# Performance work log

Measured on AMD Instinct MI355X. Metric: run time of the kernel, lower is better.

## Reference

```python
import jax, jax.numpy as jnp
import numpy as np

NUM_HEADS = 16
NEG = -1e10


def setup_inputs() -> dict:
    key = jax.random.key(0)
    ks = jax.random.split(key, 5)
    S, E = 2048, 2048
    scale_in = 1.0 / np.sqrt(E)
    return {
        "x": jax.random.normal(ks[0], (S, E), dtype=jnp.float32),
        "W_attn": jax.random.normal(ks[1], (E, 3 * E), dtype=jnp.float32) * scale_in,
        "b_attn": jax.random.normal(ks[2], (3 * E,), dtype=jnp.float32) * 0.02,
        "W_proj": jax.random.normal(ks[3], (E, E), dtype=jnp.float32) * scale_in,
        "b_proj": jax.random.normal(ks[4], (E,), dtype=jnp.float32) * 0.02,
    }


def reference(x, W_attn, b_attn, W_proj, b_proj):
    S, E = x.shape
    H = NUM_HEADS
    D = E // H
    # c_attn: [S, 3E]
    h = x @ W_attn + b_attn
    # view(S, 3, -1).transpose(0,1) -> [3, S, E]; then view(3, S, H, D).transpose(1,2) -> [3, H, S, D]
    qkv = h.reshape(S, 3, E).transpose(1, 0, 2)          # [3, S, E]
    q, k, v = qkv.reshape(3, S, H, D).transpose(0, 2, 1, 3)  # each [H, S, D]
    # causal mask: (1 - tril) * -1e10, added before softmax
    mask = (1.0 - jnp.tril(jnp.ones((S, S), dtype=x.dtype))) * NEG
    scores = jnp.einsum("hsd,htd->hst", q, k) / jnp.sqrt(jnp.asarray(D, dtype=x.dtype))
    attn = jax.nn.softmax(scores + mask, axis=-1)
    out_heads = jnp.einsum("hst,htd->hsd", attn, v)      # [H, S, D]
    # hstack over heads == transpose to [S, H, D] then flatten to [S, E]
    concat = out_heads.transpose(1, 0, 2).reshape(S, E)
    out = concat @ W_proj + b_proj
    # current_cache = (k, v) pre-head-split: [S, E] each
    return out, qkv[1], qkv[2]
```

## Files before the change

### kernel.cpp

```cpp
#include <hip/hip_runtime.h>
#include <hip/hip_bf16.h>
#include <stdint.h>

#define S_DIM 2048
#define E_DIM 2048
#define H_NUM 16
#define D_HEAD 128
#define N3E 6144

typedef __attribute__((ext_vector_type(8))) short short8;
typedef __attribute__((ext_vector_type(4))) float f32x4;
typedef __attribute__((ext_vector_type(8))) unsigned short ushort8;

__device__ __forceinline__ unsigned short f32_to_bf16_bits(float f) {
    __hip_bfloat16 b = __float2bfloat16(f);
    unsigned short u;
    __builtin_memcpy(&u, &b, 2);
    return u;
}
__device__ __forceinline__ float bf16_bits_to_f32(unsigned short u) {
    unsigned int v = ((unsigned int)u) << 16;
    float f;
    __builtin_memcpy(&f, &v, 4);
    return f;
}

__global__ void k_convert(const float* __restrict__ in, __hip_bfloat16* __restrict__ out, int n) {
    int i = (blockIdx.x * 256 + threadIdx.x) * 8;
    if (i >= n) return;
    float4 a = *(const float4*)(in + i);
    float4 b = *(const float4*)(in + i + 4);
    ushort8 o;
    o[0] = f32_to_bf16_bits(a.x);
    o[1] = f32_to_bf16_bits(a.y);
    o[2] = f32_to_bf16_bits(a.z);
    o[3] = f32_to_bf16_bits(a.w);
    o[4] = f32_to_bf16_bits(b.x);
    o[5] = f32_to_bf16_bits(b.y);
    o[6] = f32_to_bf16_bits(b.z);
    o[7] = f32_to_bf16_bits(b.w);
    *(ushort8*)(out + i) = o;
}

__global__ void k_transpose_convert(const float* __restrict__ in, __hip_bfloat16* __restrict__ out,
                                    int R, int C) {
    __shared__ float tile[32][33];
    int c0 = blockIdx.x * 32, r0 = blockIdx.y * 32;
    int tx = threadIdx.x, ty = threadIdx.y;
#pragma unroll
    for (int i = 0; i < 4; ++i) {
        int r = r0 + ty + i * 8;
        tile[ty + i * 8][tx] = in[(size_t)r * C + c0 + tx];
    }
    __syncthreads();
#pragma unroll
    for (int i = 0; i < 4; ++i) {
        int c = c0 + ty + i * 8;
        out[(size_t)c * R + r0 + tx] = __float2bfloat16(tile[tx][ty + i * 8]);
    }
}

__global__ void k_transpose_v(const __hip_bfloat16* __restrict__ qkv, __hip_bfloat16* __restrict__ vT) {
    __shared__ __hip_bfloat16 tile[32][33];
    int c0 = blockIdx.x * 32, t0 = blockIdx.y * 32;
    int tx = threadIdx.x, ty = threadIdx.y;
#pragma unroll
    for (int i = 0; i < 4; ++i) {
        int t = t0 + ty + i * 8;
        tile[ty + i * 8][tx] = qkv[(size_t)t * N3E + 2 * E_DIM + c0 + tx];
    }
    __syncthreads();
#pragma unroll
    for (int i = 0; i < 4; ++i) {
        int c = c0 + ty + i * 8;
        vT[(size_t)c * S_DIM + t0 + tx] = tile[tx][ty + i * 8];
    }
}

template <int EPI>
__global__ __launch_bounds__(512, 2) void k_gemm256(const __hip_bfloat16* __restrict__ A,
                                                    const __hip_bfloat16* __restrict__ Bt,
                                                    const float* __restrict__ bias,
                                                    float* __restrict__ outF,
                                                    __hip_bfloat16* __restrict__ outB,
                                                    int M, int N, int K) {
    __shared__ __hip_bfloat16 As[4][256 * 32];
    __shared__ __hip_bfloat16 Bs[4][256 * 32];

    const int tid = threadIdx.x;
    const int w = tid >> 6, lane = tid & 63;
    const int lg = lane >> 4, l16 = lane & 15;
    const int wr = w >> 2, wc = w & 3;
    const int ntx = N >> 8;
    const int chunk = ((M >> 8) * ntx) >> 3;
    const int lin = blockIdx.x;
    const int swz = (lin & 7) * chunk + (lin >> 3);
    const int m0 = (swz / ntx) << 8, n0 = (swz % ntx) << 8;
    const int NT = K >> 5;

    const int srow = tid >> 2;
    const int scol = ((tid & 3) ^ ((tid >> 3) & 3)) * 8;
    const __hip_bfloat16* aB = A + (size_t)(m0 + srow) * K + scol;
    const __hip_bfloat16* bB = Bt + (size_t)(n0 + srow) * K + scol;
    const size_t rstep = (size_t)128 * K;

#define STAGE(u, p)                                                                                   \
    do {                                                                                              \
        __builtin_amdgcn_global_load_lds(                                                             \
            (const __attribute__((address_space(1))) void*)(aB + (p) * rstep + (u) * 32),             \
            (__attribute__((address_space(3))) void*)(&As[(u) & 3][(p) * 4096 + tid * 8]), 16, 0, 0); \
        __builtin_amdgcn_global_load_lds(                                                             \
            (const __attribute__((address_space(1))) void*)(bB + (p) * rstep + (u) * 32),             \
            (__attribute__((address_space(3))) void*)(&Bs[(u) & 3][(p) * 4096 + tid * 8]), 16, 0, 0); \
    } while (0)

    f32x4 acc[8][4];
#pragma unroll
    for (int i = 0; i < 8; ++i)
#pragma unroll
        for (int j = 0; j < 4; ++j) acc[i][j] = {0.f, 0.f, 0.f, 0.f};

    STAGE(0, 0); STAGE(0, 1);
    STAGE(1, 0); STAGE(1, 1);
    STAGE(2, 0); STAGE(2, 1);
    asm volatile("s_waitcnt vmcnt(8)" ::: "memory");
    __builtin_amdgcn_s_barrier();

    short8 af[4], bf[4];
    for (int t = 0; t < NT; ++t) {
        const int cur = t & 3;
        const int u = t + 3;
#pragma unroll
        for (int i = 0; i < 4; ++i) {
            int arow = wr * 128 + i * 16 + l16;
            af[i] = *(const short8*)&As[cur][arow * 32 + ((lg ^ ((arow >> 1) & 3)) * 8)];
            int brow = wc * 64 + i * 16 + l16;
            bf[i] = *(const short8*)&Bs[cur][brow * 32 + ((lg ^ ((brow >> 1) & 3)) * 8)];
        }
        if (u < NT) { STAGE(u, 0); STAGE(u, 1); }
        __builtin_amdgcn_s_setprio(1);
#pragma unroll
        for (int mi = 0; mi < 4; ++mi)
#pragma unroll
            for (int ni = 0; ni < 4; ++ni)
                acc[mi][ni] = __builtin_amdgcn_mfma_f32_16x16x32_bf16(af[mi], bf[ni], acc[mi][ni], 0, 0, 0);
        __builtin_amdgcn_s_setprio(0);
#pragma unroll
        for (int i = 0; i < 4; ++i) {
            int arow = wr * 128 + 64 + i * 16 + l16;
            af[i] = *(const short8*)&As[cur][arow * 32 + ((lg ^ ((arow >> 1) & 3)) * 8)];
        }
        __builtin_amdgcn_s_setprio(1);
#pragma unroll
        for (int mi = 0; mi < 4; ++mi)
#pragma unroll
            for (int ni = 0; ni < 4; ++ni)
                acc[4 + mi][ni] = __builtin_amdgcn_mfma_f32_16x16x32_bf16(af[mi], bf[ni], acc[4 + mi][ni], 0, 0, 0);
        __builtin_amdgcn_s_setprio(0);
        __builtin_amdgcn_sched_barrier(0);
        if (t < NT - 3)
            asm volatile("s_waitcnt vmcnt(8)" ::: "memory");
        else if (t == NT - 3)
            asm volatile("s_waitcnt vmcnt(4)" ::: "memory");
        else if (t == NT - 2)
            asm volatile("s_waitcnt vmcnt(0)" ::: "memory");
        __builtin_amdgcn_sched_barrier(0);
        __builtin_amdgcn_s_barrier();
    }
#undef STAGE

    const size_t OFF_K = (size_t)S_DIM * E_DIM;
    const size_t OFF_V = 2 * (size_t)S_DIM * E_DIM;
#pragma unroll
    for (int ni = 0; ni < 4; ++ni) {
        int jcol = n0 + wc * 64 + ni * 16 + l16;
        float bj = bias[jcol];
#pragma unroll
        for (int mi = 0; mi < 8; ++mi) {
#pragma unroll
            for (int r = 0; r < 4; ++r) {
                int s = m0 + wr * 128 + mi * 16 + lg * 4 + r;
                float v = acc[mi][ni][r] + bj;
                if (EPI == 1) {
                    outB[(size_t)s * N + jcol] = __float2bfloat16(v);
                    if (jcol >= 2 * E_DIM) {
                        outF[OFF_V + (size_t)s * E_DIM + (jcol - 2 * E_DIM)] = v;
                    } else if (jcol >= E_DIM) {
                        outF[OFF_K + (size_t)s * E_DIM + (jcol - E_DIM)] = v;
                    }
                } else {
                    outF[(size_t)s * N + jcol] = v;
                }
            }
        }
    }
}

template <int EPI>
__global__ __launch_bounds__(256, 2) void k_gemm128(const __hip_bfloat16* __restrict__ A,
                                                    const __hip_bfloat16* __restrict__ Bt,
                                                    const float* __restrict__ bias,
                                                    float* __restrict__ outF,
                                                    __hip_bfloat16* __restrict__ outB,
                                                    int M, int N, int K) {
    __shared__ __hip_bfloat16 As[4][128 * 32];
    __shared__ __hip_bfloat16 Bs[4][128 * 32];

    const int tid = threadIdx.x;
    const int w = tid >> 6, lane = tid & 63;
    const int lg = lane >> 4, l16 = lane & 15;
    const int wr = w >> 1, wc = w & 1;
    const int ntx = N >> 7;
    const int chunk = ((M >> 7) * ntx) >> 3;
    const int lin = blockIdx.x;
    const int swz = (lin & 7) * chunk + (lin >> 3);
    const int m0 = (swz / ntx) << 7, n0 = (swz % ntx) << 7;
    const int NT = K >> 5;

    const int srow = tid >> 2;
    const int scol = ((tid & 3) ^ ((tid >> 3) & 3)) * 8;
    const __hip_bfloat16* aB = A + (size_t)(m0 + srow) * K + scol;
    const __hip_bfloat16* bB = Bt + (size_t)(n0 + srow) * K + scol;
    const size_t rstep = (size_t)64 * K;

#define STG(u, p)                                                                                     \
    do {                                                                                              \
        __builtin_amdgcn_global_load_lds(                                                             \
            (const __attribute__((address_space(1))) void*)(aB + (p) * rstep + (u) * 32),             \
            (__attribute__((address_space(3))) void*)(&As[(u) & 3][(p) * 2048 + tid * 8]), 16, 0, 0); \
        __builtin_amdgcn_global_load_lds(                                                             \
            (const __attribute__((address_space(1))) void*)(bB + (p) * rstep + (u) * 32),             \
            (__attribute__((address_space(3))) void*)(&Bs[(u) & 3][(p) * 2048 + tid * 8]), 16, 0, 0); \
    } while (0)

    f32x4 acc[4][4];
#pragma unroll
    for (int i = 0; i < 4; ++i)
#pragma unroll
        for (int j = 0; j < 4; ++j) acc[i][j] = {0.f, 0.f, 0.f, 0.f};

    STG(0, 0); STG(0, 1);
    STG(1, 0); STG(1, 1);
    STG(2, 0); STG(2, 1);
    asm volatile("s_waitcnt vmcnt(8)" ::: "memory");
    __builtin_amdgcn_s_barrier();

    short8 af[4], bfr[4];
    for (int t = 0; t < NT; ++t) {
        const int cur = t & 3;
        const int u = t + 3;
#pragma unroll
        for (int i = 0; i < 4; ++i) {
            int arow = wr * 64 + i * 16 + l16;
            af[i] = *(const short8*)&As[cur][arow * 32 + ((lg ^ ((arow >> 1) & 3)) * 8)];
            int brow = wc * 64 + i * 16 + l16;
            bfr[i] = *(const short8*)&Bs[cur][brow * 32 + ((lg ^ ((brow >> 1) & 3)) * 8)];
        }
        if (u < NT) { STG(u, 0); STG(u, 1); }
        __builtin_amdgcn_s_setprio(1);
#pragma unroll
        for (int mi = 0; mi < 4; ++mi)
#pragma unroll
            for (int ni = 0; ni < 4; ++ni)
                acc[mi][ni] = __builtin_amdgcn_mfma_f32_16x16x32_bf16(af[mi], bfr[ni], acc[mi][ni], 0, 0, 0);
        __builtin_amdgcn_s_setprio(0);
        __builtin_amdgcn_sched_barrier(0);
        if (t < NT - 3)
            asm volatile("s_waitcnt vmcnt(8)" ::: "memory");
        else if (t == NT - 3)
            asm volatile("s_waitcnt vmcnt(4)" ::: "memory");
        else if (t == NT - 2)
            asm volatile("s_waitcnt vmcnt(0)" ::: "memory");
        __builtin_amdgcn_sched_barrier(0);
        __builtin_amdgcn_s_barrier();
    }
#undef STG

    const size_t OFF_K = (size_t)S_DIM * E_DIM;
    const size_t OFF_V = 2 * (size_t)S_DIM * E_DIM;
#pragma unroll
    for (int ni = 0; ni < 4; ++ni) {
        int jcol = n0 + wc * 64 + ni * 16 + l16;
        float bj = bias[jcol];
#pragma unroll
        for (int mi = 0; mi < 4; ++mi) {
#pragma unroll
            for (int r = 0; r < 4; ++r) {
                int s = m0 + wr * 64 + mi * 16 + lg * 4 + r;
                float v = acc[mi][ni][r] + bj;
                if (EPI == 1) {
                    outB[(size_t)s * N + jcol] = __float2bfloat16(v);
                    if (jcol >= 2 * E_DIM) {
                        outF[OFF_V + (size_t)s * E_DIM + (jcol - 2 * E_DIM)] = v;
                    } else if (jcol >= E_DIM) {
                        outF[OFF_K + (size_t)s * E_DIM + (jcol - E_DIM)] = v;
                    }
                } else {
                    outF[(size_t)s * N + jcol] = v;
                }
            }
        }
    }
}

__global__ __launch_bounds__(256) void k_attn(const __hip_bfloat16* __restrict__ qkv,
                                              const __hip_bfloat16* __restrict__ vT,
                                              __hip_bfloat16* __restrict__ concat,
                                              __hip_bfloat16* __restrict__ Ob,
                                              float* __restrict__ ml) {
    const int h = blockIdx.y;
    const int xs = 47 - (int)blockIdx.x;
    int x, tstart, tend, chunk = 0;
    bool split;
    if (xs < 16) {
        x = xs; tstart = 0; tend = x + 1; split = false;
    } else {
        int idx = xs - 16;
        x = 16 + (idx >> 1);
        chunk = idx & 1;
        int L = x + 1, half = L >> 1;
        tstart = chunk ? half : 0;
        tend = chunk ? L : half;
        split = true;
    }
    const int q0 = x * 64;
    const int tid = threadIdx.x;
    const int w = tid >> 6, lane = tid & 63;
    const int lg = lane >> 4, l16 = lane & 15;
    const int sbase = q0 + w * 16;
    const float scale = 0.08838834764831845f;
    const float FIXM = 8.0f;

    __shared__ __hip_bfloat16 Ks[2][64 * 128];
    __shared__ __hip_bfloat16 Vs[2][128 * 64];
    __shared__ __hip_bfloat16 plds[4][16 * 84];

    short8 qa[4];
#pragma unroll
    for (int kc = 0; kc < 4; ++kc)
        qa[kc] = *(const short8*)&qkv[(size_t)(sbase + l16) * N3E + h * D_HEAD + kc * 32 + lg * 8];

    short8 ones;
#pragma unroll
    for (int j = 0; j < 8; ++j) ones[j] = (short)0x3F80;

    f32x4 O[8];
#pragma unroll
    for (int i = 0; i < 8; ++i) O[i] = {0.f, 0.f, 0.f, 0.f};
    f32x4 accL = {0.f, 0.f, 0.f, 0.f};

    auto stage = [&](int buf, int it) {
        const int t0 = it * 64;
#pragma unroll
        for (int j = 0; j < 4; ++j) {
            int kr = j * 16 + w * 4 + (lane >> 4);
            int ks16 = (lane & 15) ^ (kr & 7);
            const __hip_bfloat16* gk = qkv + (size_t)(t0 + kr) * N3E + E_DIM + h * D_HEAD + ks16 * 8;
            __builtin_amdgcn_global_load_lds((const __attribute__((address_space(1))) void*)gk,
                                             (__attribute__((address_space(3))) void*)(&Ks[buf][j * 2048 + w * 512]),
                                             16, 0, 0);
            int vd = j * 32 + w * 8 + (lane >> 3);
            int vs16 = (lane & 7) ^ (vd & 7);
            const __hip_bfloat16* gv = vT + (size_t)(h * D_HEAD + vd) * S_DIM + t0 + vs16 * 8;
            __builtin_amdgcn_global_load_lds((const __attribute__((address_space(1))) void*)gv,
                                             (__attribute__((address_space(3))) void*)(&Vs[buf][j * 2048 + w * 512]),
                                             16, 0, 0);
        }
    };

    stage(0, tstart);
    int cur = 0;

    for (int it = tstart; it < tend; ++it) {
        const int t0 = it * 64;
        __syncthreads();
        if (it + 1 < tend) stage(cur ^ 1, it + 1);
        const bool diag = (t0 == q0);

        f32x4 sc[4];
        __builtin_amdgcn_s_setprio(1);
#pragma unroll
        for (int f = 0; f < 4; ++f) {
            sc[f] = {0.f, 0.f, 0.f, 0.f};
            int r = f * 16 + l16;
#pragma unroll
            for (int kc = 0; kc < 4; ++kc) {
                int ce = (kc * 32 + lg * 8) ^ ((r & 7) << 3);
                short8 kb = *(const short8*)&Ks[cur][r * 128 + ce];
                sc[f] = __builtin_amdgcn_mfma_f32_16x16x32_bf16(qa[kc], kb, sc[f], 0, 0, 0);
            }
        }
        __builtin_amdgcn_s_setprio(0);

#pragma unroll
        for (int f = 0; f < 4; ++f) {
#pragma unroll
            for (int r = 0; r < 4; ++r) {
                float v = sc[f][r] * scale - FIXM;
                if (diag) {
                    int t = t0 + f * 16 + l16;
                    int s = sbase + lg * 4 + r;
                    if (t > s) v = -1e30f;
                }
                sc[f][r] = __expf(v);
            }
        }

#pragma unroll
        for (int f = 0; f < 4; ++f)
#pragma unroll
            for (int r = 0; r < 4; ++r)
                plds[w][(lg * 4 + r) * 84 + f * 16 + l16] = __float2bfloat16(sc[f][r]);
        short8 pa[2];
#pragma unroll
        for (int tc = 0; tc < 2; ++tc)
            pa[tc] = *(const short8*)&plds[w][l16 * 84 + tc * 32 + lg * 8];

        __builtin_amdgcn_s_setprio(1);
        accL = __builtin_amdgcn_mfma_f32_16x16x32_bf16(pa[0], ones, accL, 0, 0, 0);
        accL = __builtin_amdgcn_mfma_f32_16x16x32_bf16(pa[1], ones, accL, 0, 0, 0);
#pragma unroll
        for (int f2 = 0; f2 < 8; ++f2) {
            int d = f2 * 16 + l16;
#pragma unroll
            for (int tc = 0; tc < 2; ++tc) {
                int ce = (tc * 32 + lg * 8) ^ ((d & 7) << 3);
                short8 vb = *(const short8*)&Vs[cur][d * 64 + ce];
                O[f2] = __builtin_amdgcn_mfma_f32_16x16x32_bf16(pa[tc], vb, O[f2], 0, 0, 0);
            }
        }
        __builtin_amdgcn_s_setprio(0);
        cur ^= 1;
    }

    if (!split) {
#pragma unroll
        for (int f2 = 0; f2 < 8; ++f2) {
#pragma unroll
            for (int r = 0; r < 4; ++r) {
                int s = sbase + lg * 4 + r;
                float v = O[f2][r] / accL[r];
                concat[(size_t)s * E_DIM + h * D_HEAD + f2 * 16 + l16] = __float2bfloat16(v);
            }
        }
    } else {
        const int sub = (h * 16 + (x - 16)) * 2 + chunk;
#pragma unroll
        for (int f2 = 0; f2 < 8; ++f2) {
#pragma unroll
            for (int r = 0; r < 4; ++r) {
                int row = w * 16 + lg * 4 + r;
                Ob[(size_t)sub * 8192 + row * 128 + f2 * 16 + l16] = __float2bfloat16(O[f2][r]);
            }
        }
        if (l16 == 0) {
#pragma unroll
            for (int r = 0; r < 4; ++r) {
                int row = w * 16 + lg * 4 + r;
                ml[((size_t)sub * 64 + row) * 2 + 0] = FIXM;
                ml[((size_t)sub * 64 + row) * 2 + 1] = accL[r];
            }
        }
    }
}

__global__ __launch_bounds__(256) void k_combine(const __hip_bfloat16* __restrict__ Ob,
                                                 const float* __restrict__ ml,
                                                 __hip_bfloat16* __restrict__ concat) {
    const int xx = blockIdx.x;
    const int h = blockIdx.y;
    const int tid = threadIdx.x;
    const int row = tid >> 2;
    const int d0 = (tid & 3) * 32;
    const int sub0 = (h * 16 + xx) * 2, sub1 = sub0 + 1;
    const float m0 = ml[((size_t)sub0 * 64 + row) * 2 + 0];
    const float l0 = ml[((size_t)sub0 * 64 + row) * 2 + 1];
    const float m1 = ml[((size_t)sub1 * 64 + row) * 2 + 0];
    const float l1 = ml[((size_t)sub1 * 64 + row) * 2 + 1];
    const float M = fmaxf(m0, m1);
    const float w0 = __expf(m0 - M), w1 = __expf(m1 - M);
    const float inv = 1.f / (w0 * l0 + w1 * l1);
    const int s = (xx + 16) * 64 + row;
#pragma unroll
    for (int j = 0; j < 32; j += 8) {
        ushort8 a = *(const ushort8*)&Ob[(size_t)sub0 * 8192 + row * 128 + d0 + j];
        ushort8 b = *(const ushort8*)&Ob[(size_t)sub1 * 8192 + row * 128 + d0 + j];
        ushort8 o;
#pragma unroll
        for (int q = 0; q < 8; ++q) {
            float fa = bf16_bits_to_f32(a[q]);
            float fb = bf16_bits_to_f32(b[q]);
            o[q] = f32_to_bf16_bits((w0 * fa + w1 * fb) * inv);
        }
        *(ushort8*)&concat[(size_t)s * E_DIM + h * D_HEAD + d0 + j] = o;
    }
}

extern "C" void kernel_launch(void* const* d_in, const int* in_sizes, int n_in,
                              void* d_out, int out_size, void* d_ws, size_t ws_size,
                              hipStream_t stream) {
    const float* x = (const float*)d_in[0];
    const float* W_attn = (const float*)d_in[1];
    const float* b_attn = (const float*)d_in[2];
    const float* W_proj = (const float*)d_in[3];
    const float* b_proj = (const float*)d_in[4];
    float* out = (float*)d_out;

    __hip_bfloat16* xb = (__hip_bfloat16*)d_ws;
    __hip_bfloat16* WaT = xb + (size_t)S_DIM * E_DIM;
    __hip_bfloat16* WpT = WaT + (size_t)N3E * E_DIM;
    __hip_bfloat16* qkvb = WpT + (size_t)E_DIM * E_DIM;
    __hip_bfloat16* vT = qkvb + (size_t)S_DIM * N3E;
    __hip_bfloat16* concat = xb;
    __hip_bfloat16* Ob = WaT;
    float* ml = (float*)(WaT + (size_t)512 * 8192);

    k_convert<<<dim3((S_DIM * E_DIM) / (256 * 8)), dim3(256), 0, stream>>>(x, xb, S_DIM * E_DIM);
    k_transpose_convert<<<dim3(N3E / 32, E_DIM / 32), dim3(32, 8), 0, stream>>>(W_attn, WaT, E_DIM, N3E);
    k_transpose_convert<<<dim3(E_DIM / 32, E_DIM / 32), dim3(32, 8), 0, stream>>>(W_proj, WpT, E_DIM, E_DIM);
    k_gemm256<1><<<dim3(192), dim3(512), 0, stream>>>(xb, WaT, b_attn, out, qkvb, S_DIM, N3E, E_DIM);
    k_transpose_v<<<dim3(E_DIM / 32, S_DIM / 32), dim3(32, 8), 0, stream>>>(qkvb, vT);
    k_attn<<<dim3(48, H_NUM), dim3(256), 0, stream>>>(qkvb, vT, concat, Ob, ml);
    k_combine<<<dim3(16, H_NUM), dim3(256), 0, stream>>>(Ob, ml, concat);
    k_gemm128<0><<<dim3(256), dim3(256), 0, stream>>>(concat, WpT, b_proj, out, nullptr,
                                                      S_DIM, E_DIM, E_DIM);
}
```

Before: 206.3 us.

## Restructure QKV GEMM into double-buffered 64-wide K steps with split A/B staging

Rewrites the pipeline of the 256x256 QKV projection GEMM. The 4-deep ring of 32-wide K tiles becomes a double buffer of 64-wide K tiles split into two halves. A and B prefetches are interleaved between four MFMA sub-phases, each separated by barriers, and the 2D launch grid replaces the swizzled 1D block order. The aim is better overlap of global-to-LDS loads with MFMA work and deeper per-iteration compute. It adds many more barriers per iteration and drops the L2-friendly tile swizzle, which could hurt cache reuse.

```diff
diff --git a/kernel.cpp b/kernel.cpp
--- a/kernel.cpp
+++ b/kernel.cpp
@@ -11,6 +11,10 @@
 typedef __attribute__((ext_vector_type(8))) short short8;
 typedef __attribute__((ext_vector_type(4))) float f32x4;
 typedef __attribute__((ext_vector_type(8))) unsigned short ushort8;
+
+#define GLD16(src, dst)                                                          \
+    __builtin_amdgcn_global_load_lds((const __attribute__((address_space(1))) void*)(src), \
+                                     (__attribute__((address_space(3))) void*)(dst), 16, 0, 0)
 
 __device__ __forceinline__ unsigned short f32_to_bf16_bits(float f) {
     __hip_bfloat16 b = __float2bfloat16(f);
@@ -84,35 +88,38 @@
                                                     float* __restrict__ outF,
                                                     __hip_bfloat16* __restrict__ outB,
                                                     int M, int N, int K) {
-    __shared__ __hip_bfloat16 As[4][256 * 32];
-    __shared__ __hip_bfloat16 Bs[4][256 * 32];
+    __shared__ __hip_bfloat16 As[2][2][256 * 32];
+    __shared__ __hip_bfloat16 Bs[2][2][256 * 32];
 
     const int tid = threadIdx.x;
     const int w = tid >> 6, lane = tid & 63;
     const int lg = lane >> 4, l16 = lane & 15;
     const int wr = w >> 2, wc = w & 3;
-    const int ntx = N >> 8;
-    const int chunk = ((M >> 8) * ntx) >> 3;
-    const int lin = blockIdx.x;
-    const int swz = (lin & 7) * chunk + (lin >> 3);
-    const int m0 = (swz / ntx) << 8, n0 = (swz % ntx) << 8;
-    const int NT = K >> 5;
-
-    const int srow = tid >> 2;
-    const int scol = ((tid & 3) ^ ((tid >> 3) & 3)) * 8;
-    const __hip_bfloat16* aB = A + (size_t)(m0 + srow) * K + scol;
-    const __hip_bfloat16* bB = Bt + (size_t)(n0 + srow) * K + scol;
-    const size_t rstep = (size_t)128 * K;
-
-#define STAGE(u, p)                                                                                   \
-    do {                                                                                              \
-        __builtin_amdgcn_global_load_lds(                                                             \
-            (const __attribute__((address_space(1))) void*)(aB + (p) * rstep + (u) * 32),             \
-            (__attribute__((address_space(3))) void*)(&As[(u) & 3][(p) * 4096 + tid * 8]), 16, 0, 0); \
-        __builtin_amdgcn_global_load_lds(                                                             \
-            (const __attribute__((address_space(1))) void*)(bB + (p) * rstep + (u) * 32),             \
-            (__attribute__((address_space(3))) void*)(&Bs[(u) & 3][(p) * 4096 + tid * 8]), 16, 0, 0); \
-    } while (0)
+    const int m0 = blockIdx.y * 256, n0 = blockIdx.x * 256;
+    const int NT = K >> 6;
+
+    int srow[2], sk16[2];
+#pragma unroll
+    for (int j = 0; j < 2; ++j) {
+        int slot = j * 512 + tid;
+        srow[j] = slot >> 2;
+        sk16[j] = (tid & 3) ^ ((slot >> 3) & 3);
+    }
+
+    auto stageA = [&](int buf, int kh, int t) {
+#pragma unroll
+        for (int j = 0; j < 2; ++j) {
+            const __hip_bfloat16* g = A + (size_t)(m0 + srow[j]) * K + t * 64 + kh * 32 + sk16[j] * 8;
+            GLD16(g, &As[buf][kh][(j * 512 + tid) * 8]);
+        }
+    };
+    auto stageB = [&](int buf, int kh, int t) {
+#pragma unroll
+        for (int j = 0; j < 2; ++j) {
+            const __hip_bfloat16* g = Bt + (size_t)(n0 + srow[j]) * K + t * 64 + kh * 32 + sk16[j] * 8;
+            GLD16(g, &Bs[buf][kh][(j * 512 + tid) * 8]);
+        }
+    };
 
     f32x4 acc[8][4];
 #pragma unroll
@@ -120,54 +127,107 @@
 #pragma unroll
         for (int j = 0; j < 4; ++j) acc[i][j] = {0.f, 0.f, 0.f, 0.f};
 
-    STAGE(0, 0); STAGE(0, 1);
-    STAGE(1, 0); STAGE(1, 1);
-    STAGE(2, 0); STAGE(2, 1);
-    asm volatile("s_waitcnt vmcnt(8)" ::: "memory");
+    stageA(0, 0, 0);
+    stageB(0, 0, 0);
+    stageA(0, 1, 0);
+    stageB(0, 1, 0);
+    asm volatile("s_waitcnt vmcnt(4)" ::: "memory");
     __builtin_amdgcn_s_barrier();
 
-    short8 af[4], bf[4];
     for (int t = 0; t < NT; ++t) {
-        const int cur = t & 3;
-        const int u = t + 3;
-#pragma unroll
-        for (int i = 0; i < 4; ++i) {
-            int arow = wr * 128 + i * 16 + l16;
-            af[i] = *(const short8*)&As[cur][arow * 32 + ((lg ^ ((arow >> 1) & 3)) * 8)];
-            int brow = wc * 64 + i * 16 + l16;
-            bf[i] = *(const short8*)&Bs[cur][brow * 32 + ((lg ^ ((brow >> 1) & 3)) * 8)];
-        }
-        if (u < NT) { STAGE(u, 0); STAGE(u, 1); }
-        __builtin_amdgcn_s_setprio(1);
-#pragma unroll
-        for (int mi = 0; mi < 4; ++mi)
-#pragma unroll
-            for (int ni = 0; ni < 4; ++ni)
-                acc[mi][ni] = __builtin_amdgcn_mfma_f32_16x16x32_bf16(af[mi], bf[ni], acc[mi][ni], 0, 0, 0);
-        __builtin_amdgcn_s_setprio(0);
-#pragma unroll
-        for (int i = 0; i < 4; ++i) {
-            int arow = wr * 128 + 64 + i * 16 + l16;
-            af[i] = *(const short8*)&As[cur][arow * 32 + ((lg ^ ((arow >> 1) & 3)) * 8)];
-        }
-        __builtin_amdgcn_s_setprio(1);
-#pragma unroll
-        for (int mi = 0; mi < 4; ++mi)
-#pragma unroll
-            for (int ni = 0; ni < 4; ++ni)
-                acc[4 + mi][ni] = __builtin_amdgcn_mfma_f32_16x16x32_bf16(af[mi], bf[ni], acc[4 + mi][ni], 0, 0, 0);
-        __builtin_amdgcn_s_setprio(0);
-        __builtin_amdgcn_sched_barrier(0);
-        if (t < NT - 3)
-            asm volatile("s_waitcnt vmcnt(8)" ::: "memory");
-        else if (t == NT - 3)
-            asm volatile("s_waitcnt vmcnt(4)" ::: "memory");
-        else if (t == NT - 2)
-            asm volatile("s_waitcnt vmcnt(0)" ::: "memory");
-        __builtin_amdgcn_sched_barrier(0);
-        __builtin_amdgcn_s_barrier();
-    }
-#undef STAGE
+        const int cur = t & 1;
+        const int nt = (t + 1 < NT) ? t + 1 : t;
+        const int nb = (t + 1) & 1;
+        short8 af[8], bp0[2], bp1[2];
+
+#pragma unroll
+        for (int mi = 0; mi < 8; ++mi) {
+            int row = wr * 128 + mi * 16 + l16;
+            af[mi] = *(const short8*)&As[cur][0][row * 32 + ((lg ^ ((row >> 1) & 3)) * 8)];
+        }
+#pragma unroll
+        for (int p = 0; p < 2; ++p) {
+            int row = wc * 64 + p * 16 + l16;
+            bp0[p] = *(const short8*)&Bs[cur][0][row * 32 + ((lg ^ ((row >> 1) & 3)) * 8)];
+        }
+        stageA(nb, 0, nt);
+        __builtin_amdgcn_s_barrier();
+        asm volatile("s_waitcnt lgkmcnt(0)" ::: "memory");
+        __builtin_amdgcn_sched_barrier(0);
+        __builtin_amdgcn_s_setprio(1);
+#pragma unroll
+        for (int mi = 0; mi < 8; ++mi)
+#pragma unroll
+            for (int p = 0; p < 2; ++p)
+                acc[mi][p] = __builtin_amdgcn_mfma_f32_16x16x32_bf16(af[mi], bp0[p], acc[mi][p], 0, 0, 0);
+        __builtin_amdgcn_s_setprio(0);
+        __builtin_amdgcn_s_barrier();
+
+#pragma unroll
+        for (int p = 0; p < 2; ++p) {
+            int row = wc * 64 + (2 + p) * 16 + l16;
+            bp1[p] = *(const short8*)&Bs[cur][0][row * 32 + ((lg ^ ((row >> 1) & 3)) * 8)];
+        }
+        stageB(nb, 0, nt);
+        __builtin_amdgcn_s_barrier();
+        asm volatile("s_waitcnt lgkmcnt(0)" ::: "memory");
+        __builtin_amdgcn_sched_barrier(0);
+        __builtin_amdgcn_s_setprio(1);
+#pragma unroll
+        for (int mi = 0; mi < 8; ++mi)
+#pragma unroll
+            for (int p = 0; p < 2; ++p)
+                acc[mi][2 + p] = __builtin_amdgcn_mfma_f32_16x16x32_bf16(af[mi], bp1[p], acc[mi][2 + p], 0, 0, 0);
+        __builtin_amdgcn_s_setprio(0);
+        __builtin_amdgcn_sched_barrier(0);
+        asm volatile("s_waitcnt vmcnt(4)" ::: "memory");
+        __builtin_amdgcn_sched_barrier(0);
+        __builtin_amdgcn_s_barrier();
+
+#pragma unroll
+        for (int mi = 0; mi < 8; ++mi) {
+            int row = wr * 128 + mi * 16 + l16;
+            af[mi] = *(const short8*)&As[cur][1][row * 32 + ((lg ^ ((row >> 1) & 3)) * 8)];
+        }
+#pragma unroll
+        for (int p = 0; p < 2; ++p) {
+            int row = wc * 64 + p * 16 + l16;
+            bp0[p] = *(const short8*)&Bs[cur][1][row * 32 + ((lg ^ ((row >> 1) & 3)) * 8)];
+        }
+        stageA(nb, 1, nt);
+        __builtin_amdgcn_s_barrier();
+        asm volatile("s_waitcnt lgkmcnt(0)" ::: "memory");
+        __builtin_amdgcn_sched_barrier(0);
+        __builtin_amdgcn_s_setprio(1);
+#pragma unroll
+        for (int mi = 0; mi < 8; ++mi)
+#pragma unroll
+            for (int p = 0; p < 2; ++p)
+                acc[mi][p] = __builtin_amdgcn_mfma_f32_16x16x32_bf16(af[mi], bp0[p], acc[mi][p], 0, 0, 0);
+        __builtin_amdgcn_s_setprio(0);
+        __builtin_amdgcn_s_barrier();
+
+#pragma unroll
+        for (int p = 0; p < 2; ++p) {
+            int row = wc * 64 + (2 + p) * 16 + l16;
+            bp1[p] = *(const short8*)&Bs[cur][1][row * 32 + ((lg ^ ((row >> 1) & 3)) * 8)];
+        }
+        stageB(nb, 1, nt);
+        __builtin_amdgcn_s_barrier();
+        asm volatile("s_waitcnt lgkmcnt(0)" ::: "memory");
+        __builtin_amdgcn_sched_barrier(0);
+        __builtin_amdgcn_s_setprio(1);
+#pragma unroll
+        for (int mi = 0; mi < 8; ++mi)
+#pragma unroll
+            for (int p = 0; p < 2; ++p)
+                acc[mi][2 + p] = __builtin_amdgcn_mfma_f32_16x16x32_bf16(af[mi], bp1[p], acc[mi][2 + p], 0, 0, 0);
+        __builtin_amdgcn_s_setprio(0);
+        __builtin_amdgcn_sched_barrier(0);
+        asm volatile("s_waitcnt vmcnt(4)" ::: "memory");
+        __builtin_amdgcn_sched_barrier(0);
+        __builtin_amdgcn_s_barrier();
+    }
 
     const size_t OFF_K = (size_t)S_DIM * E_DIM;
     const size_t OFF_V = 2 * (size_t)S_DIM * E_DIM;
@@ -225,12 +285,8 @@
 
 #define STG(u, p)                                                                                     \
     do {                                                                                              \
-        __builtin_amdgcn_global_load_lds(                                                             \
-            (const __attribute__((address_space(1))) void*)(aB + (p) * rstep + (u) * 32),             \
-            (__attribute__((address_space(3))) void*)(&As[(u) & 3][(p) * 2048 + tid * 8]), 16, 0, 0); \
-        __builtin_amdgcn_global_load_lds(                                                             \
-            (const __attribute__((address_space(1))) void*)(bB + (p) * rstep + (u) * 32),             \
-            (__attribute__((address_space(3))) void*)(&Bs[(u) & 3][(p) * 2048 + tid * 8]), 16, 0, 0); \
+        GLD16(aB + (p) * rstep + (u) * 32, &As[(u) & 3][(p) * 2048 + tid * 8]);                       \
+        GLD16(bB + (p) * rstep + (u) * 32, &Bs[(u) & 3][(p) * 2048 + tid * 8]);                       \
     } while (0)
 
     f32x4 acc[4][4];
@@ -356,15 +412,11 @@
             int kr = j * 16 + w * 4 + (lane >> 4);
             int ks16 = (lane & 15) ^ (kr & 7);
             const __hip_bfloat16* gk = qkv + (size_t)(t0 + kr) * N3E + E_DIM + h * D_HEAD + ks16 * 8;
-            __builtin_amdgcn_global_load_lds((const __attribute__((address_space(1))) void*)gk,
-                                             (__attribute__((address_space(3))) void*)(&Ks[buf][j * 2048 + w * 512]),
-                                             16, 0, 0);
+            GLD16(gk, &Ks[buf][j * 2048 + w * 512]);
             int vd = j * 32 + w * 8 + (lane >> 3);
             int vs16 = (lane & 7) ^ (vd & 7);
             const __hip_bfloat16* gv = vT + (size_t)(h * D_HEAD + vd) * S_DIM + t0 + vs16 * 8;
-            __builtin_amdgcn_global_load_lds((const __attribute__((address_space(1))) void*)gv,
-                                             (__attribute__((address_space(3))) void*)(&Vs[buf][j * 2048 + w * 512]),
-                                             16, 0, 0);
+            GLD16(gv, &Vs[buf][j * 2048 + w * 512]);
         }
     };
 
@@ -518,7 +570,8 @@
     k_convert<<<dim3((S_DIM * E_DIM) / (256 * 8)), dim3(256), 0, stream>>>(x, xb, S_DIM * E_DIM);
     k_transpose_convert<<<dim3(N3E / 32, E_DIM / 32), dim3(32, 8), 0, stream>>>(W_attn, WaT, E_DIM, N3E);
     k_transpose_convert<<<dim3(E_DIM / 32, E_DIM / 32), dim3(32, 8), 0, stream>>>(W_proj, WpT, E_DIM, E_DIM);
-    k_gemm256<1><<<dim3(192), dim3(512), 0, stream>>>(xb, WaT, b_attn, out, qkvb, S_DIM, N3E, E_DIM);
+    k_gemm256<1><<<dim3(N3E / 256, S_DIM / 256), dim3(512), 0, stream>>>(xb, WaT, b_attn, out, qkvb,
+                                                                         S_DIM, N3E, E_DIM);
     k_transpose_v<<<dim3(E_DIM / 32, S_DIM / 32), dim3(32, 8), 0, stream>>>(qkvb, vT);
     k_attn<<<dim3(48, H_NUM), dim3(256), 0, stream>>>(qkvb, vT, concat, Ob, ml);
     k_combine<<<dim3(16, H_NUM), dim3(256), 0, stream>>>(Ob, ml, concat);
```

After: 196.4 us. 4.8% less time.
